# Performance work log

Hardware: AMD Instinct MI355X
Metric: run time of the kernel (lower is better)

## Reference

```python
import jax, jax.numpy as jnp
import numpy as np

EPS = 1e-8


def _dtw_distance(cost):
    """Classic DTW DP: D[i,j] = cost[i,j] + min(D[i-1,j], D[i-1,j-1], D[i,j-1]).
    Rows are processed with lax.scan; the within-row left-to-right recurrence
    D[j] = min(a[j], D[j-1] + c[j]) is solved in closed form as a min-plus scan:
    with S = cumsum(c), D = cummin(a - S) + S.
    """
    # first row: only horizontal moves -> running cumsum
    d0 = jnp.cumsum(cost[0])

    def row_step(prev, c):
        # prev: D[i-1, :]  (shape [m]);  c: cost[i, :]
        prev_diag = jnp.concatenate([jnp.full((1,), jnp.inf, prev.dtype), prev[:-1]])
        a = c + jnp.minimum(prev, prev_diag)          # candidate from above / diagonal
        S = jnp.cumsum(c)
        d = jax.lax.cummin(a - S) + S                 # folds in the left-neighbor path
        return d, None

    d_last, _ = jax.lax.scan(row_step, d0, cost[1:])
    return d_last[-1]


def setup_inputs() -> dict:
    key = jax.random.key(0)
    k1, k2 = jax.random.split(key)
    N1, N2, D = 4096, 4096, 1024
    return {
        "trajectory1": jax.random.normal(k1, (N1, D), dtype=jnp.float32),
        "trajectory2": jax.random.normal(k2, (N2, D), dtype=jnp.float32),
    }


def reference(trajectory1, trajectory2):
    # cosine distance matrix: 1 - <t1_hat, t2_hat>
    t1 = trajectory1 / (jnp.linalg.norm(trajectory1, axis=-1, keepdims=True) + EPS)
    t2 = trajectory2 / (jnp.linalg.norm(trajectory2, axis=-1, keepdims=True) + EPS)
    cost = 1.0 - jnp.einsum('id,jd->ij', t1, t2)      # [N1, N2]
    distance = _dtw_distance(cost)
    similarity = 1.0 / (1.0 + distance)
    return similarity
```

## Files before the change

kernel.cpp:

```cpp
#include <hip/hip_runtime.h>
#include <hip/hip_bf16.h>
#include <stdint.h>

#define KDIM 1024
#define NROW 4096
#define NCOL 4096
#define INFV 1e30f
#define INFBITS 0x7149F2CAu
#define BM 128
#define BK 32

#define SKROWS 4160
#define NBLK32 130
#define DLAG   16
#define EMAX   190

typedef __bf16 bf16x8 __attribute__((ext_vector_type(8)));
typedef float f32x4 __attribute__((ext_vector_type(4)));

#define CFENCE asm volatile("" ::: "memory")

__device__ __forceinline__ unsigned short f2bf(float f) {
    __hip_bfloat16 h = __float2bfloat16(f);
    return *reinterpret_cast<unsigned short*>(&h);
}

__device__ __forceinline__ void gll16(const void* gsrc, void* ldst) {
    __builtin_amdgcn_global_load_lds(
        (const __attribute__((address_space(1))) void*)gsrc,
        (__attribute__((address_space(3))) void*)ldst, 16, 0, 0);
}

__global__ __launch_bounds__(256) void normalize_bf16(
    const float* __restrict__ t1, const float* __restrict__ t2,
    unsigned short* __restrict__ o1, unsigned short* __restrict__ o2)
{
    int b = blockIdx.x;
    int t = threadIdx.x;
    const float* src;
    unsigned short* dst;
    if (b < NROW) { src = t1 + (size_t)b * KDIM;          dst = o1 + (size_t)b * KDIM; }
    else          { src = t2 + (size_t)(b - NROW) * KDIM; dst = o2 + (size_t)(b - NROW) * KDIM; }

    float4 v = reinterpret_cast<const float4*>(src)[t];
    float ss = v.x * v.x + v.y * v.y + v.z * v.z + v.w * v.w;
    #pragma unroll
    for (int d = 32; d >= 1; d >>= 1) ss += __shfl_xor(ss, d, 64);

    __shared__ float wsum[4];
    int wave = t >> 6;
    if ((t & 63) == 0) wsum[wave] = ss;
    __syncthreads();
    float inv = 1.0f / (sqrtf(wsum[0] + wsum[1] + wsum[2] + wsum[3]) + 1e-8f);

    ushort4 o;
    o.x = f2bf(v.x * inv);
    o.y = f2bf(v.y * inv);
    o.z = f2bf(v.z * inv);
    o.w = f2bf(v.w * inv);
    reinterpret_cast<ushort4*>(dst)[t] = o;
}

__global__ __launch_bounds__(256) void gemm_cost(
    const unsigned short* __restrict__ A,
    const unsigned short* __restrict__ B,
    unsigned short* __restrict__ Cs)
{
    __shared__ __align__(16) unsigned short As[BM * BK];
    __shared__ __align__(16) unsigned short Bs[BM * BK];

    int t    = threadIdx.x;
    int lane = t & 63;
    int wave = t >> 6;
    int i0   = blockIdx.y * BM;
    int j0   = blockIdx.x * BM;

    f32x4 acc[4][4];
    f32x4 zero = {0.f, 0.f, 0.f, 0.f};
    #pragma unroll
    for (int m = 0; m < 4; ++m)
        #pragma unroll
        for (int n = 0; n < 4; ++n) acc[m][n] = zero;

    int frow = lane & 15;
    int fk   = (lane >> 4) * 8;
    int wr   = (wave >> 1) * 64;
    int wc   = (wave & 1) * 64;

    int srow = t >> 2;
    int scb  = (t & 3) * 8;

    uint4 ra0, ra1, rb0, rb1;
    {
        ra0 = *reinterpret_cast<const uint4*>(A + (size_t)(i0 + srow) * KDIM + scb);
        ra1 = *reinterpret_cast<const uint4*>(A + (size_t)(i0 + 64 + srow) * KDIM + scb);
        rb0 = *reinterpret_cast<const uint4*>(B + (size_t)(j0 + srow) * KDIM + scb);
        rb1 = *reinterpret_cast<const uint4*>(B + (size_t)(j0 + 64 + srow) * KDIM + scb);
    }

    for (int k0 = 0; k0 < KDIM; k0 += BK) {
        __syncthreads();
        *reinterpret_cast<uint4*>(As + (size_t)t * 8)         = ra0;
        *reinterpret_cast<uint4*>(As + (size_t)(256 + t) * 8) = ra1;
        *reinterpret_cast<uint4*>(Bs + (size_t)t * 8)         = rb0;
        *reinterpret_cast<uint4*>(Bs + (size_t)(256 + t) * 8) = rb1;
        __syncthreads();

        if (k0 + BK < KDIM) {
            int kn = k0 + BK;
            ra0 = *reinterpret_cast<const uint4*>(A + (size_t)(i0 + srow) * KDIM + kn + scb);
            ra1 = *reinterpret_cast<const uint4*>(A + (size_t)(i0 + 64 + srow) * KDIM + kn + scb);
            rb0 = *reinterpret_cast<const uint4*>(B + (size_t)(j0 + srow) * KDIM + kn + scb);
            rb1 = *reinterpret_cast<const uint4*>(B + (size_t)(j0 + 64 + srow) * KDIM + kn + scb);
        }

        bf16x8 af[4], bfr[4];
        #pragma unroll
        for (int m = 0; m < 4; ++m)
            af[m] = *reinterpret_cast<const bf16x8*>(As + (wr + m * 16 + frow) * BK + fk);
        #pragma unroll
        for (int n = 0; n < 4; ++n)
            bfr[n] = *reinterpret_cast<const bf16x8*>(Bs + (wc + n * 16 + frow) * BK + fk);

        #pragma unroll
        for (int m = 0; m < 4; ++m)
            #pragma unroll
            for (int n = 0; n < 4; ++n)
                acc[m][n] = __builtin_amdgcn_mfma_f32_16x16x32_bf16(af[m], bfr[n], acc[m][n], 0, 0, 0);
    }

    int crow = (lane >> 4) * 4;
    int ccol = lane & 15;
    #pragma unroll
    for (int n = 0; n < 4; ++n) {
        const int j  = j0 + wc + n * 16 + ccol;
        const int Lj = (j >> 2) & 63;
        #pragma unroll
        for (int m = 0; m < 4; ++m) {
            const int ibase = i0 + wr + m * 16 + crow;
            #pragma unroll
            for (int q = 0; q < 4; ++q)
                Cs[(size_t)(ibase + q + Lj) * NCOL + j] = f2bf(1.0f - acc[m][n][q]);
        }
    }
}

__global__ __launch_bounds__(256, 1) void dtw_systolic(
    const unsigned short* __restrict__ cost,
    unsigned long long* __restrict__ ring,
    float* __restrict__ out)
{
    __shared__ __align__(16) unsigned char clds[4 * 2 * 16384];
    __shared__ float outRow[4][128];
    __shared__ float outRowD[4][64];

    const int w    = blockIdx.x;
    const int tid  = threadIdx.x;
    const int v    = tid >> 6;
    const int lane = tid & 63;
    const int stripe = 4 * w + v;
    const bool gCon  = (v == 0 && w > 0);
    const bool gPro  = (v == 3 && w < 3);
    const bool first = (stripe == 0);
    const char* skewb = (const char*)cost;
    const unsigned long long* rseg = ring + (size_t)(w > 0 ? w - 1 : 0) * 4096;
    unsigned long long* wseg = ring + (size_t)w * 4096;
    unsigned long long* garb = ring + (size_t)3 * 4096 + w * 64;
    const unsigned l32 = (unsigned)(lane & 31);
    const unsigned stripeByte = (unsigned)stripe * 512u + ((unsigned)(lane & 31) << 4);
    unsigned char* myclds = clds + v * 32768;

    float pd0 = INFV, pd1 = INFV, pd2 = INFV, pd3 = INFV;
    float lprev = (first && lane == 0) ? 0.0f : INFV;
    float d3p = INFV;
    unsigned ansb = INFBITS;
    unsigned long long rv0 = 0;

#define GLL16S(STG) { int sg_ = (STG); sg_ = sg_ < 0 ? 0 : (sg_ > NBLK32 - 1 ? NBLK32 - 1 : sg_); \
    unsigned char* ldsb_ = myclds + (sg_ & 1) * 16384; \
    _Pragma("unroll") \
    for (int g_ = 0; g_ < 16; ++g_) { \
        int sr_ = 32 * sg_ + 2 * g_ + (lane >> 5); \
        if (sr_ > SKROWS - 1) sr_ = SKROWS - 1; \
        gll16(skewb + (size_t)sr_ * 8192 + stripeByte, ldsb_ + g_ * 1024); } }

#define RINGLD(DST, BI) { int pb_ = (BI); pb_ = pb_ < 0 ? 0 : (pb_ > 127 ? 127 : pb_); \
    const unsigned off_ = (32u * (unsigned)pb_ + l32) * 8u; \
    asm volatile("global_load_dwordx2 %0, %1, %2 sc0 sc1" \
                 : "=v"(DST) : "v"(off_), "s"(rseg) : "memory"); }

#define DCOMP(K, CU) { \
    const unsigned rbK = (unsigned)__builtin_amdgcn_readlane(rvhi, (K)); \
    const float lcur = __uint_as_float((unsigned)__builtin_amdgcn_update_dpp( \
        (int)rbK, (int)__float_as_uint(d3p), 0x138, 0xf, 0xf, false)); \
    const float c0 = __uint_as_float(CU.x << 16); \
    const float c1 = __uint_as_float(CU.x & 0xffff0000u); \
    const float c2 = __uint_as_float(CU.y << 16); \
    const float c3 = __uint_as_float(CU.y & 0xffff0000u); \
    const float n0 = c0 + fminf(pd0, lprev); \
    const float n1 = c1 + fminf(pd1, pd0); \
    const float n2 = c2 + fminf(pd2, pd1); \
    const float n3 = c3 + fminf(pd3, pd2); \
    const float e0 = fminf(lcur + c0, n0); \
    const float e1 = fminf(e0 + c1, n1); \
    const float e2 = fminf(e1 + c2, n2); \
    const float e3 = fminf(e2 + c3, n3); \
    float* sp_ = (lane == 63) ? &outRow[v][(unsigned)(rowbase + (K)) & 127u] \
                              : &outRowD[v][lane]; \
    *sp_ = e3; \
    ansb = (tjb + (K) == 4158) ? __float_as_uint(e3) : ansb; \
    lprev = lcur; d3p = e3; \
    pd0 = e0; pd1 = e1; pd2 = e2; pd3 = e3; }

    if (v == 0) {
        GLL16S(0)
        if (gCon) RINGLD(rv0, 0)
    }

    #pragma unroll 1
    for (int e = 0; e < EMAX; ++e) {
        CFENCE;
        asm volatile("s_waitcnt lgkmcnt(0)" ::: "memory");
        __builtin_amdgcn_s_barrier();
        CFENCE;

        const int ib = e - 3 * v - DLAG * w;

        GLL16S(ib + 1)
        unsigned long long rvN = 0;
        if (gCon) RINGLD(rvN, ib + 1)

        if (gCon) {
            asm volatile("s_waitcnt vmcnt(17)" : "+v"(rv0) :: "memory");
        } else if (gPro) {
            asm volatile("s_waitcnt vmcnt(17)" ::: "memory");
        } else {
            asm volatile("s_waitcnt vmcnt(16)" ::: "memory");
        }

        if (ib >= 0 && ib < NBLK32) {
            const uint2* lu = reinterpret_cast<const uint2*>(
                myclds + (ib & 1) * 16384 + (lane << 3));
            const uint2 cc0  = lu[0 * 64],  cc1  = lu[1 * 64];
            const uint2 cc2  = lu[2 * 64],  cc3  = lu[3 * 64];
            const uint2 cc4  = lu[4 * 64],  cc5  = lu[5 * 64];
            const uint2 cc6  = lu[6 * 64],  cc7  = lu[7 * 64];
            const uint2 cc8  = lu[8 * 64],  cc9  = lu[9 * 64];
            const uint2 cc10 = lu[10 * 64], cc11 = lu[11 * 64];
            const uint2 cc12 = lu[12 * 64], cc13 = lu[13 * 64];
            const uint2 cc14 = lu[14 * 64], cc15 = lu[15 * 64];
            const uint2 cc16 = lu[16 * 64], cc17 = lu[17 * 64];
            const uint2 cc18 = lu[18 * 64], cc19 = lu[19 * 64];
            const uint2 cc20 = lu[20 * 64], cc21 = lu[21 * 64];
            const uint2 cc22 = lu[22 * 64], cc23 = lu[23 * 64];
            const uint2 cc24 = lu[24 * 64], cc25 = lu[25 * 64];
            const uint2 cc26 = lu[26 * 64], cc27 = lu[27 * 64];
            const uint2 cc28 = lu[28 * 64], cc29 = lu[29 * 64];
            const uint2 cc30 = lu[30 * 64], cc31 = lu[31 * 64];

            int rvhi;
            if (gCon) {
                if (ib < 128) {
                    const unsigned expt = 32u * (unsigned)ib + l32 + 1u;
                    while (__ballot((unsigned)rv0 == expt) != ~0ull)
                        rv0 = __hip_atomic_load(rseg + 32u * (unsigned)ib + l32,
                                                __ATOMIC_RELAXED, __HIP_MEMORY_SCOPE_AGENT);
                }
                rvhi = (int)(unsigned)(rv0 >> 32);
            } else if (v > 0) {
                rvhi = (int)__float_as_uint(
                    outRow[v - 1][(32u * (unsigned)ib + l32) & 127u]);
            } else {
                rvhi = (int)INFBITS;
            }

            const int rowbase = 32 * ib - 63;
            const int tjb = 32 * ib;

            DCOMP(0,  cc0)  DCOMP(1,  cc1)  DCOMP(2,  cc2)  DCOMP(3,  cc3)
            DCOMP(4,  cc4)  DCOMP(5,  cc5)  DCOMP(6,  cc6)  DCOMP(7,  cc7)
            DCOMP(8,  cc8)  DCOMP(9,  cc9)  DCOMP(10, cc10) DCOMP(11, cc11)
            DCOMP(12, cc12) DCOMP(13, cc13) DCOMP(14, cc14) DCOMP(15, cc15)
            DCOMP(16, cc16) DCOMP(17, cc17) DCOMP(18, cc18) DCOMP(19, cc19)
            DCOMP(20, cc20) DCOMP(21, cc21) DCOMP(22, cc22) DCOMP(23, cc23)
            DCOMP(24, cc24) DCOMP(25, cc25) DCOMP(26, cc26) DCOMP(27, cc27)
            DCOMP(28, cc28) DCOMP(29, cc29) DCOMP(30, cc30) DCOMP(31, cc31)
        }

        if (gPro) {
            const int r = 32 * ib - 63 + (int)l32;
            const float bv = outRow[3][(unsigned)r & 127u];
            const bool valid = (lane < 32) && (ib >= 0) && (ib < NBLK32) &&
                               (r >= 0) && (r <= 4095);
            if (lane < 32) {
                const unsigned long long pk =
                    ((unsigned long long)__float_as_uint(bv) << 32) | (unsigned)(r + 1);
                unsigned long long* sp = valid ? (wseg + r) : (garb + lane);
                (void)__hip_atomic_exchange(sp, pk, __ATOMIC_RELAXED,
                                            __HIP_MEMORY_SCOPE_AGENT);
            }
        }

        rv0 = rvN;
    }

#undef GLL16S
#undef RINGLD
#undef DCOMP

    if (stripe == 15 && lane == 63) out[0] = 1.0f / (1.0f + __uint_as_float(ansb));
}

extern "C" void kernel_launch(void* const* d_in, const int* in_sizes, int n_in,
                              void* d_out, int out_size, void* d_ws, size_t ws_size,
                              hipStream_t stream)
{
    const float* t1 = (const float*)d_in[0];
    const float* t2 = (const float*)d_in[1];
    float* out = (float*)d_out;

    char* ws = (char*)d_ws;
    unsigned short* t1n  = (unsigned short*)ws;
    unsigned short* t2n  = (unsigned short*)(ws + (size_t)NROW * KDIM * 2);
    unsigned short* skew = (unsigned short*)(ws + (size_t)16 * 1024 * 1024);
    unsigned long long* ring = (unsigned long long*)(ws + (size_t)52 * 1024 * 1024);

    hipMemsetAsync(ring, 0, (size_t)(3 * 4096 + 4 * 64) * 8, stream);
    normalize_bf16<<<2 * NROW, 256, 0, stream>>>(t1, t2, t1n, t2n);
    gemm_cost<<<dim3(NCOL / BM, NROW / BM), 256, 0, stream>>>(t1n, t2n, skew);
    dtw_systolic<<<4, 256, 0, stream>>>(skew, ring, out);
}
```

Before: 600.8 us.

## Split DTW systolic into 16 single-wave workgroups linked by global rings

Replaces the 4-workgroup by 4-wave DTW wavefront, which synchronized waves through LDS with block barriers and a fixed lag schedule, with 16 independent single-wave workgroups. Each one owns a column stripe and passes its boundary column to the next through a global ring buffer using flag-tagged atomics. Ring loads are prefetched three blocks ahead so the spin-wait is less likely to stall. A small init kernel seeds a dummy infinite-valued ring for the first workgroup. The intent is to remove per-step block barriers and idle skew steps, at the cost of more cross-CU global-memory handoffs, each with its own latency.

Measured after the change: 517.0 us. 1.16x faster.

```diff
diff --git a/kernel.cpp b/kernel.cpp
--- a/kernel.cpp
+++ b/kernel.cpp
@@ -12,8 +12,7 @@
 
 #define SKROWS 4160
 #define NBLK32 130
-#define DLAG   16
-#define EMAX   190
+#define NWG    16
 
 typedef __bf16 bf16x8 __attribute__((ext_vector_type(8)));
 typedef float f32x4 __attribute__((ext_vector_type(4)));
@@ -145,39 +144,40 @@
     }
 }
 
-__global__ __launch_bounds__(256, 1) void dtw_systolic(
+__global__ __launch_bounds__(256) void ring_init(unsigned long long* __restrict__ ring)
+{
+    int i = blockIdx.x * 256 + threadIdx.x;
+    ring[(size_t)15 * NROW + i] =
+        ((unsigned long long)INFBITS << 32) | (unsigned)(i + 1);
+}
+
+__global__ __launch_bounds__(64, 1) void dtw_systolic(
     const unsigned short* __restrict__ cost,
     unsigned long long* __restrict__ ring,
     float* __restrict__ out)
 {
-    __shared__ __align__(16) unsigned char clds[4 * 2 * 16384];
-    __shared__ float outRow[4][128];
-    __shared__ float outRowD[4][64];
+    __shared__ __align__(16) unsigned char clds[2 * 16384];
+    __shared__ float outT[32];
+    __shared__ float outD[64];
 
     const int w    = blockIdx.x;
-    const int tid  = threadIdx.x;
-    const int v    = tid >> 6;
-    const int lane = tid & 63;
-    const int stripe = 4 * w + v;
-    const bool gCon  = (v == 0 && w > 0);
-    const bool gPro  = (v == 3 && w < 3);
-    const bool first = (stripe == 0);
+    const int lane = threadIdx.x;
     const char* skewb = (const char*)cost;
-    const unsigned long long* rseg = ring + (size_t)(w > 0 ? w - 1 : 0) * 4096;
-    unsigned long long* wseg = ring + (size_t)w * 4096;
-    unsigned long long* garb = ring + (size_t)3 * 4096 + w * 64;
+    const unsigned long long* rseg = ring + (size_t)((w == 0) ? 15 : (w - 1)) * NROW;
+    unsigned long long* wseg = (w < NWG - 1) ? (ring + (size_t)w * NROW)
+                                             : (ring + (size_t)NWG * NROW + w * 64);
+    unsigned long long* garb = ring + (size_t)NWG * NROW + w * 64;
     const unsigned l32 = (unsigned)(lane & 31);
-    const unsigned stripeByte = (unsigned)stripe * 512u + ((unsigned)(lane & 31) << 4);
-    unsigned char* myclds = clds + v * 32768;
+    const unsigned stripeByte = (unsigned)w * 512u + ((unsigned)(lane & 31) << 4);
 
     float pd0 = INFV, pd1 = INFV, pd2 = INFV, pd3 = INFV;
-    float lprev = (first && lane == 0) ? 0.0f : INFV;
+    float lprev = (w == 0 && lane == 0) ? 0.0f : INFV;
     float d3p = INFV;
     unsigned ansb = INFBITS;
-    unsigned long long rv0 = 0;
+    unsigned long long rv0 = 0, rv1 = 0, rv2 = 0;
 
 #define GLL16S(STG) { int sg_ = (STG); sg_ = sg_ < 0 ? 0 : (sg_ > NBLK32 - 1 ? NBLK32 - 1 : sg_); \
-    unsigned char* ldsb_ = myclds + (sg_ & 1) * 16384; \
+    unsigned char* ldsb_ = clds + (sg_ & 1) * 16384; \
     _Pragma("unroll") \
     for (int g_ = 0; g_ < 16; ++g_) { \
         int sr_ = 32 * sg_ + 2 * g_ + (lane >> 5); \
@@ -205,93 +205,68 @@
     const float e1 = fminf(e0 + c1, n1); \
     const float e2 = fminf(e1 + c2, n2); \
     const float e3 = fminf(e2 + c3, n3); \
-    float* sp_ = (lane == 63) ? &outRow[v][(unsigned)(rowbase + (K)) & 127u] \
-                              : &outRowD[v][lane]; \
+    float* sp_ = (lane == 63) ? &outT[K] : &outD[lane]; \
     *sp_ = e3; \
     ansb = (tjb + (K) == 4158) ? __float_as_uint(e3) : ansb; \
     lprev = lcur; d3p = e3; \
     pd0 = e0; pd1 = e1; pd2 = e2; pd3 = e3; }
 
-    if (v == 0) {
-        GLL16S(0)
-        if (gCon) RINGLD(rv0, 0)
-    }
+    GLL16S(0)
+    RINGLD(rv0, 0) RINGLD(rv1, 1) RINGLD(rv2, 2)
+    CFENCE;
 
     #pragma unroll 1
-    for (int e = 0; e < EMAX; ++e) {
+    for (int ib = 0; ib < NBLK32; ++ib) {
+        GLL16S(ib + 1)
+        unsigned long long rvN;
+        RINGLD(rvN, ib + 3)
         CFENCE;
-        asm volatile("s_waitcnt lgkmcnt(0)" ::: "memory");
-        __builtin_amdgcn_s_barrier();
-        CFENCE;
-
-        const int ib = e - 3 * v - DLAG * w;
-
-        GLL16S(ib + 1)
-        unsigned long long rvN = 0;
-        if (gCon) RINGLD(rvN, ib + 1)
-
-        if (gCon) {
-            asm volatile("s_waitcnt vmcnt(17)" : "+v"(rv0) :: "memory");
-        } else if (gPro) {
-            asm volatile("s_waitcnt vmcnt(17)" ::: "memory");
-        } else {
-            asm volatile("s_waitcnt vmcnt(16)" ::: "memory");
+        asm volatile("s_waitcnt vmcnt(19)" : "+v"(rv0) :: "memory");
+
+        if (ib < 128) {
+            const unsigned expt = 32u * (unsigned)ib + l32 + 1u;
+            while (__ballot((unsigned)rv0 == expt) != ~0ull)
+                rv0 = __hip_atomic_load(rseg + 32u * (unsigned)ib + l32,
+                                        __ATOMIC_RELAXED, __HIP_MEMORY_SCOPE_AGENT);
         }
-
-        if (ib >= 0 && ib < NBLK32) {
-            const uint2* lu = reinterpret_cast<const uint2*>(
-                myclds + (ib & 1) * 16384 + (lane << 3));
-            const uint2 cc0  = lu[0 * 64],  cc1  = lu[1 * 64];
-            const uint2 cc2  = lu[2 * 64],  cc3  = lu[3 * 64];
-            const uint2 cc4  = lu[4 * 64],  cc5  = lu[5 * 64];
-            const uint2 cc6  = lu[6 * 64],  cc7  = lu[7 * 64];
-            const uint2 cc8  = lu[8 * 64],  cc9  = lu[9 * 64];
-            const uint2 cc10 = lu[10 * 64], cc11 = lu[11 * 64];
-            const uint2 cc12 = lu[12 * 64], cc13 = lu[13 * 64];
-            const uint2 cc14 = lu[14 * 64], cc15 = lu[15 * 64];
-            const uint2 cc16 = lu[16 * 64], cc17 = lu[17 * 64];
-            const uint2 cc18 = lu[18 * 64], cc19 = lu[19 * 64];
-            const uint2 cc20 = lu[20 * 64], cc21 = lu[21 * 64];
-            const uint2 cc22 = lu[22 * 64], cc23 = lu[23 * 64];
-            const uint2 cc24 = lu[24 * 64], cc25 = lu[25 * 64];
-            const uint2 cc26 = lu[26 * 64], cc27 = lu[27 * 64];
-            const uint2 cc28 = lu[28 * 64], cc29 = lu[29 * 64];
-            const uint2 cc30 = lu[30 * 64], cc31 = lu[31 * 64];
-
-            int rvhi;
-            if (gCon) {
-                if (ib < 128) {
-                    const unsigned expt = 32u * (unsigned)ib + l32 + 1u;
-                    while (__ballot((unsigned)rv0 == expt) != ~0ull)
-                        rv0 = __hip_atomic_load(rseg + 32u * (unsigned)ib + l32,
-                                                __ATOMIC_RELAXED, __HIP_MEMORY_SCOPE_AGENT);
-                }
-                rvhi = (int)(unsigned)(rv0 >> 32);
-            } else if (v > 0) {
-                rvhi = (int)__float_as_uint(
-                    outRow[v - 1][(32u * (unsigned)ib + l32) & 127u]);
-            } else {
-                rvhi = (int)INFBITS;
-            }
-
-            const int rowbase = 32 * ib - 63;
-            const int tjb = 32 * ib;
-
-            DCOMP(0,  cc0)  DCOMP(1,  cc1)  DCOMP(2,  cc2)  DCOMP(3,  cc3)
-            DCOMP(4,  cc4)  DCOMP(5,  cc5)  DCOMP(6,  cc6)  DCOMP(7,  cc7)
-            DCOMP(8,  cc8)  DCOMP(9,  cc9)  DCOMP(10, cc10) DCOMP(11, cc11)
-            DCOMP(12, cc12) DCOMP(13, cc13) DCOMP(14, cc14) DCOMP(15, cc15)
-            DCOMP(16, cc16) DCOMP(17, cc17) DCOMP(18, cc18) DCOMP(19, cc19)
-            DCOMP(20, cc20) DCOMP(21, cc21) DCOMP(22, cc22) DCOMP(23, cc23)
-            DCOMP(24, cc24) DCOMP(25, cc25) DCOMP(26, cc26) DCOMP(27, cc27)
-            DCOMP(28, cc28) DCOMP(29, cc29) DCOMP(30, cc30) DCOMP(31, cc31)
-        }
-
-        if (gPro) {
-            const int r = 32 * ib - 63 + (int)l32;
-            const float bv = outRow[3][(unsigned)r & 127u];
-            const bool valid = (lane < 32) && (ib >= 0) && (ib < NBLK32) &&
-                               (r >= 0) && (r <= 4095);
+        const int rvhi = (int)(unsigned)(rv0 >> 32);
+
+        const uint2* lu = reinterpret_cast<const uint2*>(
+            clds + (ib & 1) * 16384 + (lane << 3));
+        const uint2 cc0  = lu[0 * 64],  cc1  = lu[1 * 64];
+        const uint2 cc2  = lu[2 * 64],  cc3  = lu[3 * 64];
+        const uint2 cc4  = lu[4 * 64],  cc5  = lu[5 * 64];
+        const uint2 cc6  = lu[6 * 64],  cc7  = lu[7 * 64];
+        const uint2 cc8  = lu[8 * 64],  cc9  = lu[9 * 64];
+        const uint2 cc10 = lu[10 * 64], cc11 = lu[11 * 64];
+        const uint2 cc12 = lu[12 * 64], cc13 = lu[13 * 64];
+        const uint2 cc14 = lu[14 * 64], cc15 = lu[15 * 64];
+        const uint2 cc16 = lu[16 * 64], cc17 = lu[17 * 64];
+        const uint2 cc18 = lu[18 * 64], cc19 = lu[19 * 64];
+        const uint2 cc20 = lu[20 * 64], cc21 = lu[21 * 64];
+        const uint2 cc22 = lu[22 * 64], cc23 = lu[23 * 64];
+        const uint2 cc24 = lu[24 * 64], cc25 = lu[25 * 64];
+        const uint2 cc26 = lu[26 * 64], cc27 = lu[27 * 64];
+        const uint2 cc28 = lu[28 * 64], cc29 = lu[29 * 64];
+        const uint2 cc30 = lu[30 * 64], cc31 = lu[31 * 64];
+
+        const int rowbase = 32 * ib - 63;
+        const int tjb = 32 * ib;
+
+        DCOMP(0,  cc0)  DCOMP(1,  cc1)  DCOMP(2,  cc2)  DCOMP(3,  cc3)
+        DCOMP(4,  cc4)  DCOMP(5,  cc5)  DCOMP(6,  cc6)  DCOMP(7,  cc7)
+        DCOMP(8,  cc8)  DCOMP(9,  cc9)  DCOMP(10, cc10) DCOMP(11, cc11)
+        DCOMP(12, cc12) DCOMP(13, cc13) DCOMP(14, cc14) DCOMP(15, cc15)
+        DCOMP(16, cc16) DCOMP(17, cc17) DCOMP(18, cc18) DCOMP(19, cc19)
+        DCOMP(20, cc20) DCOMP(21, cc21) DCOMP(22, cc22) DCOMP(23, cc23)
+        DCOMP(24, cc24) DCOMP(25, cc25) DCOMP(26, cc26) DCOMP(27, cc27)
+        DCOMP(28, cc28) DCOMP(29, cc29) DCOMP(30, cc30) DCOMP(31, cc31)
+
+        {
+            const float bv = outT[l32];
+            const int r = rowbase + (int)l32;
+            const bool valid = (lane < 32) && (r >= 0) && (r <= 4095) &&
+                               (w < NWG - 1);
             if (lane < 32) {
                 const unsigned long long pk =
                     ((unsigned long long)__float_as_uint(bv) << 32) | (unsigned)(r + 1);
@@ -300,15 +275,16 @@
                                             __HIP_MEMORY_SCOPE_AGENT);
             }
         }
-
-        rv0 = rvN;
+        CFENCE;
+
+        rv0 = rv1; rv1 = rv2; rv2 = rvN;
     }
 
 #undef GLL16S
 #undef RINGLD
 #undef DCOMP
 
-    if (stripe == 15 && lane == 63) out[0] = 1.0f / (1.0f + __uint_as_float(ansb));
+    if (w == NWG - 1 && lane == 63) out[0] = 1.0f / (1.0f + __uint_as_float(ansb));
 }
 
 extern "C" void kernel_launch(void* const* d_in, const int* in_sizes, int n_in,
@@ -325,8 +301,9 @@
     unsigned short* skew = (unsigned short*)(ws + (size_t)16 * 1024 * 1024);
     unsigned long long* ring = (unsigned long long*)(ws + (size_t)52 * 1024 * 1024);
 
-    hipMemsetAsync(ring, 0, (size_t)(3 * 4096 + 4 * 64) * 8, stream);
+    hipMemsetAsync(ring, 0, (size_t)15 * NROW * 8, stream);
+    ring_init<<<NROW / 256, 256, 0, stream>>>(ring);
     normalize_bf16<<<2 * NROW, 256, 0, stream>>>(t1, t2, t1n, t2n);
     gemm_cost<<<dim3(NCOL / BM, NROW / BM), 256, 0, stream>>>(t1n, t2n, skew);
-    dtw_systolic<<<4, 256, 0, stream>>>(skew, ring, out);
-}
+    dtw_systolic<<<NWG, 64, 0, stream>>>(skew, ring, out);
+}
```
